# Kernel tuning notes

Hardware: AMD Instinct MI355X
Metric: run time of the kernel (lower is better)

The kernel has to match this reference:

```python
import jax, jax.numpy as jnp
import numpy as np

CHANNEL_N = 16
RESET_PROB = 0.5
ALIVE_THRESH = 0.1


def _perceive_kernel(c):
    # Faithful reproduction of the TF kernel construction:
    # stack([sobel_x, sobel_y, identity], axis=0) -> (3,3,3); expand_dims(-2);
    # repeat over channels -> (3,3,C,3). Depthwise conv treats axis0 as filter
    # height and the last axis as the channel multiplier (same as tf code).
    sx = jnp.array([[-1.0, 0.0, 1.0], [-2.0, 0.0, 2.0], [-1.0, 0.0, 1.0]], jnp.float32) / 8.0
    sy = sx.T
    ident = jnp.zeros((3, 3), jnp.float32).at[1, 1].set(1.0)
    k = jnp.stack([sx, sy, ident], axis=0)          # (3,3,3)
    k = jnp.repeat(k[:, :, None, :], c, axis=2)     # (3,3,C,3)
    # TF depthwise output ordering: out_ch = c*multiplier + m -> flatten (C,3)
    return k.reshape(3, 3, 1, c * 3)                # HWIO for grouped conv


def _alive_mask(x):
    # 3x3 max-pool (stride 1, SAME) on alpha channel, thresholded.
    alpha = x[..., 3:4]
    pooled = jax.lax.reduce_window(alpha, -jnp.inf, jax.lax.max,
                                   (1, 3, 3, 1), (1, 1, 1, 1), 'SAME')
    return pooled > ALIVE_THRESH


def setup_inputs() -> dict:
    key = jax.random.key(0)
    k1, k2, k3, k4, k5, k6 = jax.random.split(key, 6)
    B, H, W, C = 32, 256, 256, CHANNEL_N
    x = jax.random.uniform(k1, (B, H, W, C), dtype=jnp.float32)
    rand_mask = jax.random.uniform(k2, (B, H, W, 1), dtype=jnp.float32)
    W1 = jax.random.normal(k3, (3 * C, 128), dtype=jnp.float32) * 0.1
    b1 = jax.random.normal(k4, (128,), dtype=jnp.float32) * 0.1
    W2 = jax.random.normal(k5, (128, C), dtype=jnp.float32) * 0.1
    b2 = jax.random.normal(k6, (C,), dtype=jnp.float32) * 0.1
    return {"x": x, "rand_mask": rand_mask, "W1": W1, "b1": b1, "W2": W2, "b2": b2}


def reference(x, rand_mask, W1, b1, W2, b2):
    C = x.shape[-1]
    pre_update_mask = _alive_mask(x)
    # perceive: depthwise stencil conv, multiplier 3 -> (N,H,W,3C)
    kern = _perceive_kernel(C)
    y = jax.lax.conv_general_dilated(
        x, kern, window_strides=(1, 1), padding='SAME',
        dimension_numbers=('NHWC', 'HWIO', 'NHWC'), feature_group_count=C)
    # rule model: per-cell 1x1 MLP
    h = jax.nn.relu(jnp.einsum('nhwk,kd->nhwd', y, W1) + b1)
    dx = jnp.einsum('nhwd,dc->nhwc', h, W2) + b2
    # stochastic update mask
    upd = (rand_mask < RESET_PROB).astype(x.dtype)
    x = x + dx * upd
    post_update_mask = _alive_mask(x)
    life_mask = jnp.logical_and(pre_update_mask, post_update_mask).astype(x.dtype)
    return x * life_mask
```

## Files before the change

kernel.cpp:

```cpp
#include <hip/hip_runtime.h>

typedef __bf16 bf16x8 __attribute__((ext_vector_type(8)));
typedef float f32x4 __attribute__((ext_vector_type(4)));

#define XS_COLS 66
#define XS_CHP_B 32
#define XS_SLOT_B (XS_COLS * XS_CHP_B)
#define H_BYTES 16384
#define OFF_XS H_BYTES
#define SMEM_BYTES (H_BYTES + 4 * XS_SLOT_B)

__device__ __forceinline__ unsigned short bfbits(float f) {
    __bf16 b = (__bf16)f;
    return __builtin_bit_cast(unsigned short, b);
}

__global__ __launch_bounds__(256, 4) void nca_main(
    const float* __restrict__ x, const float* __restrict__ rm,
    const float* __restrict__ W1, const float* __restrict__ b1,
    const float* __restrict__ W2, const float* __restrict__ b2,
    float* __restrict__ out, unsigned int* __restrict__ am)
{
    __shared__ __align__(16) char smem[SMEM_BYTES];
    char* Hb  = smem;
    char* XSb = smem + OFF_XS;

    const int tid  = threadIdx.x;
    const int lane = tid & 63;
    const int wid  = tid >> 6;
    const int lrow = lane & 15;
    const int kg   = lane >> 4;
    const int kgh  = kg >> 1;
    const int kgl  = kg & 1;

    int raw = blockIdx.x;
    int wg  = (raw & 7) * 512 + (raw >> 3);
    int img = wg >> 7;
    int rem = wg & 127;
    int h0  = (rem >> 2) * 8;
    int w0  = (rem & 3) << 6;

    const size_t imgbase = (size_t)img * 65536;
    const int r = wid;

    bf16x8 wt[2][3];
    #pragma unroll
    for (int m = 0; m < 2; ++m) {
        int n = (r * 2 + m) * 16 + lrow;
        #pragma unroll
        for (int kk = 0; kk < 3; ++kk) {
            float c0, c1, c2;
            if (kk == 0) {
                c0 = kgh ? -0.25f : -0.125f; c1 = 0.f; c2 = kgh ? 0.25f : 0.125f;
            } else if (kk == 1) {
                c0 = -0.125f;
                c1 = kgh ? -0.25f  : 0.f;
                c2 = kgh ? -0.125f : 0.125f;
            } else {
                c0 = kgh ? 0.f : 0.125f; c1 = kgh ? 1.f : 0.25f; c2 = kgh ? 0.f : 0.125f;
            }
            bf16x8 v;
            #pragma unroll
            for (int j = 0; j < 8; ++j) {
                int ch = kgl * 8 + j;
                float wv = c0 * W1[(3 * ch + 0) * 128 + n]
                         + c1 * W1[(3 * ch + 1) * 128 + n]
                         + c2 * W1[(3 * ch + 2) * 128 + n];
                v[j] = (__bf16)wv;
            }
            wt[m][kk] = v;
        }
    }

    bf16x8 w2f[4];
    #pragma unroll
    for (int kk = 0; kk < 4; ++kk) {
        bf16x8 v;
        #pragma unroll
        for (int j = 0; j < 8; ++j)
            v[j] = (__bf16)W2[(kk * 32 + kg * 8 + j) * 16 + lrow];
        w2f[kk] = v;
    }

    f32x4 b1q[2];
    #pragma unroll
    for (int m = 0; m < 2; ++m)
        b1q[m] = *reinterpret_cast<const f32x4*>(b1 + (r * 2 + m) * 16 + kg * 4);
    const f32x4 b2q = *reinterpret_cast<const f32x4*>(b2 + kg * 4);

    for (int idx = tid; idx < 3 * 264; idx += 256) {
        int rr  = idx / 264;
        int q   = idx - rr * 264;
        int col = q >> 2, chq = q & 3;
        int gh = h0 - 1 + rr, gw = w0 + col - 1;
        int slot = (gh + 4) & 3;
        float4 v = make_float4(0.f, 0.f, 0.f, 0.f);
        if (gh >= 0 && gh < 256 && gw >= 0 && gw < 256)
            v = *reinterpret_cast<const float4*>(x + (imgbase + (size_t)gh * 256 + gw) * 16 + chq * 4);
        ushort4 qq = { bfbits(v.x), bfbits(v.y), bfbits(v.z), bfbits(v.w) };
        *reinterpret_cast<ushort4*>(XSb + slot * XS_SLOT_B + col * XS_CHP_B + chq * 8) = qq;
    }
    __syncthreads();

    for (int i = 0; i < 8; ++i) {
        int h = h0 + i;
        int sbm = ((h + 3) & 3) * XS_SLOT_B;
        int sb0 = ((h + 4) & 3) * XS_SLOT_B;
        int sbp = ((h + 5) & 3) * XS_SLOT_B;

        #pragma unroll
        for (int t = 0; t < 4; ++t) {
            int pxl = t * 16 + lrow;
            int colbase = (pxl + 1) * XS_CHP_B + kgl * 16;
            const char* a0p = XSb + sbm + colbase + (kgh ? 0 : -XS_CHP_B);
            const char* a1p = kgh ? (XSb + sb0 + colbase - XS_CHP_B) : (XSb + sbm + colbase + XS_CHP_B);
            const char* a2p = kgh ? (XSb + sbp + colbase)            : (XSb + sb0 + colbase + XS_CHP_B);
            bf16x8 bf0 = *reinterpret_cast<const bf16x8*>(a0p);
            bf16x8 bf1 = *reinterpret_cast<const bf16x8*>(a1p);
            bf16x8 bf2 = *reinterpret_cast<const bf16x8*>(a2p);
            f32x4 a0 = {0.f, 0.f, 0.f, 0.f}, a1 = {0.f, 0.f, 0.f, 0.f};
            a0 = __builtin_amdgcn_mfma_f32_16x16x32_bf16(wt[0][0], bf0, a0, 0, 0, 0);
            a1 = __builtin_amdgcn_mfma_f32_16x16x32_bf16(wt[1][0], bf0, a1, 0, 0, 0);
            a0 = __builtin_amdgcn_mfma_f32_16x16x32_bf16(wt[0][1], bf1, a0, 0, 0, 0);
            a1 = __builtin_amdgcn_mfma_f32_16x16x32_bf16(wt[1][1], bf1, a1, 0, 0, 0);
            a0 = __builtin_amdgcn_mfma_f32_16x16x32_bf16(wt[0][2], bf2, a0, 0, 0, 0);
            a1 = __builtin_amdgcn_mfma_f32_16x16x32_bf16(wt[1][2], bf2, a1, 0, 0, 0);
            #pragma unroll
            for (int m = 0; m < 2; ++m) {
                f32x4 hv = m ? a1 : a0;
                f32x4 bq = b1q[m];
                ushort4 q;
                q.x = bfbits(fmaxf(hv[0] + bq[0], 0.f));
                q.y = bfbits(fmaxf(hv[1] + bq[1], 0.f));
                q.z = bfbits(fmaxf(hv[2] + bq[2], 0.f));
                q.w = bfbits(fmaxf(hv[3] + bq[3], 0.f));
                int n0 = (r * 2 + m) * 16 + kg * 4;
                int chunk = (n0 >> 3) ^ (pxl & 7);
                *reinterpret_cast<ushort4*>(Hb + pxl * 256 + chunk * 16 + ((n0 >> 2) & 1) * 8) = q;
            }
        }
        __syncthreads();

        float4 sv0 = make_float4(0.f, 0.f, 0.f, 0.f), sv1 = make_float4(0.f, 0.f, 0.f, 0.f);
        const bool do_stage = (i < 7);
        const int gh2 = h + 2;
        if (do_stage) {
            int col0 = tid >> 2, chq0 = tid & 3;
            int gw = w0 + col0 - 1;
            if (gh2 < 256 && gw >= 0 && gw < 256)
                sv0 = *reinterpret_cast<const float4*>(x + (imgbase + (size_t)gh2 * 256 + gw) * 16 + chq0 * 4);
            if (tid < 8) {
                int col1 = 64 + (tid >> 2), gw1 = w0 + col1 - 1;
                if (gh2 < 256 && gw1 >= 0 && gw1 < 256)
                    sv1 = *reinterpret_cast<const float4*>(x + (imgbase + (size_t)gh2 * 256 + gw1) * 16 + (tid & 3) * 4);
            }
        }

        const int pxl2 = wid * 16 + lrow;
        f32x4 acc2 = {0.f, 0.f, 0.f, 0.f};
        #pragma unroll
        for (int kk = 0; kk < 4; ++kk) {
            int chunk = (4 * kk + kg) ^ (pxl2 & 7);
            bf16x8 hb = *reinterpret_cast<const bf16x8*>(Hb + pxl2 * 256 + chunk * 16);
            acc2 = __builtin_amdgcn_mfma_f32_16x16x32_bf16(w2f[kk], hb, acc2, 0, 0, 0);
        }

        size_t pix = imgbase + (size_t)h * 256 + w0 + pxl2;
        float upd = (rm[pix] < 0.5f) ? 1.f : 0.f;
        float4 xv = *reinterpret_cast<const float4*>(x + pix * 16 + kg * 4);
        float4 xn;
        xn.x = xv.x + (acc2[0] + b2q[0]) * upd;
        xn.y = xv.y + (acc2[1] + b2q[1]) * upd;
        xn.z = xv.z + (acc2[2] + b2q[2]) * upd;
        xn.w = xv.w + (acc2[3] + b2q[3]) * upd;
        *reinterpret_cast<float4*>(out + pix * 16 + kg * 4) = xn;
        if (kg == 0) {
            unsigned int av = ((unsigned int)bfbits(xv.w) << 16) | (unsigned int)bfbits(xn.w);
            am[pix] = av;
        }

        if (do_stage) {
            int slot = (gh2 + 4) & 3;
            {
                int col0 = tid >> 2, chq0 = tid & 3;
                ushort4 q = { bfbits(sv0.x), bfbits(sv0.y), bfbits(sv0.z), bfbits(sv0.w) };
                *reinterpret_cast<ushort4*>(XSb + slot * XS_SLOT_B + col0 * XS_CHP_B + chq0 * 8) = q;
            }
            if (tid < 8) {
                int col1 = 64 + (tid >> 2);
                ushort4 q = { bfbits(sv1.x), bfbits(sv1.y), bfbits(sv1.z), bfbits(sv1.w) };
                *reinterpret_cast<ushort4*>(XSb + slot * XS_SLOT_B + col1 * XS_CHP_B + (tid & 3) * 8) = q;
            }
        }
        __syncthreads();
    }
}

__global__ __launch_bounds__(256) void nca_life(
    const unsigned int* __restrict__ am, float* __restrict__ out)
{
    int q = blockIdx.x * 256 + threadIdx.x;
    int w = q & 255, hh = (q >> 8) & 255;
    float mn = -1e30f, mo = -1e30f;
    #pragma unroll
    for (int dh = -1; dh <= 1; ++dh) {
        int h2 = hh + dh;
        if (h2 < 0 || h2 > 255) continue;
        #pragma unroll
        for (int dw = -1; dw <= 1; ++dw) {
            int w2 = w + dw;
            if (w2 < 0 || w2 > 255) continue;
            unsigned int v = am[q + dh * 256 + dw];
            mn = fmaxf(mn, __uint_as_float(v << 16));
            mo = fmaxf(mo, __uint_as_float(v & 0xffff0000u));
        }
    }
    if (!(mo > 0.1f && mn > 0.1f)) {
        float4 z = make_float4(0.f, 0.f, 0.f, 0.f);
        float4* o = (float4*)(out + (size_t)q * 16);
        o[0] = z; o[1] = z; o[2] = z; o[3] = z;
    }
}

extern "C" void kernel_launch(void* const* d_in, const int* in_sizes, int n_in,
                              void* d_out, int out_size, void* d_ws, size_t ws_size,
                              hipStream_t stream) {
    (void)in_sizes; (void)n_in; (void)out_size; (void)ws_size;
    const float* x  = (const float*)d_in[0];
    const float* rm = (const float*)d_in[1];
    const float* W1 = (const float*)d_in[2];
    const float* b1 = (const float*)d_in[3];
    const float* W2 = (const float*)d_in[4];
    const float* b2 = (const float*)d_in[5];
    float* out = (float*)d_out;
    unsigned int* am = (unsigned int*)d_ws;

    nca_main<<<dim3(4096), dim3(256), 0, stream>>>(x, rm, W1, b1, W2, b2, out, am);
    nca_life<<<dim3(8192), dim3(256), 0, stream>>>(am, out);
}
```

Baseline: 127.4 us.

## Software-pipeline MLP layers with double-buffered hidden tile to halve barriers

Restructures the per-row loop so that layer 2 for row i-1 and layer 1 for row i run in the same iteration. The hidden-activation buffer is double-buffered and the x row ring grows from 4 to 8 slots, so each iteration needs one barrier instead of two. A final epilogue handles the last row. This roughly doubles the shared memory footprint to about 49KB per block, which may cut occupancy below the four blocks the launch bounds target.

Result: slower. 140.7 us (+10.5%).

```diff
diff --git a/kernel.cpp b/kernel.cpp
--- a/kernel.cpp
+++ b/kernel.cpp
@@ -6,9 +6,9 @@
 #define XS_COLS 66
 #define XS_CHP_B 32
 #define XS_SLOT_B (XS_COLS * XS_CHP_B)
-#define H_BYTES 16384
-#define OFF_XS H_BYTES
-#define SMEM_BYTES (H_BYTES + 4 * XS_SLOT_B)
+#define H_BUF_B 16384
+#define OFF_XS (2 * H_BUF_B)
+#define SMEM_BYTES (2 * H_BUF_B + 8 * XS_SLOT_B)
 
 __device__ __forceinline__ unsigned short bfbits(float f) {
     __bf16 b = (__bf16)f;
@@ -93,7 +93,7 @@
         int q   = idx - rr * 264;
         int col = q >> 2, chq = q & 3;
         int gh = h0 - 1 + rr, gw = w0 + col - 1;
-        int slot = (gh + 4) & 3;
+        int slot = (gh + 8) & 7;
         float4 v = make_float4(0.f, 0.f, 0.f, 0.f);
         if (gh >= 0 && gh < 256 && gw >= 0 && gw < 256)
             v = *reinterpret_cast<const float4*>(x + (imgbase + (size_t)gh * 256 + gw) * 16 + chq * 4);
@@ -104,46 +104,13 @@
 
     for (int i = 0; i < 8; ++i) {
         int h = h0 + i;
-        int sbm = ((h + 3) & 3) * XS_SLOT_B;
-        int sb0 = ((h + 4) & 3) * XS_SLOT_B;
-        int sbp = ((h + 5) & 3) * XS_SLOT_B;
-
-        #pragma unroll
-        for (int t = 0; t < 4; ++t) {
-            int pxl = t * 16 + lrow;
-            int colbase = (pxl + 1) * XS_CHP_B + kgl * 16;
-            const char* a0p = XSb + sbm + colbase + (kgh ? 0 : -XS_CHP_B);
-            const char* a1p = kgh ? (XSb + sb0 + colbase - XS_CHP_B) : (XSb + sbm + colbase + XS_CHP_B);
-            const char* a2p = kgh ? (XSb + sbp + colbase)            : (XSb + sb0 + colbase + XS_CHP_B);
-            bf16x8 bf0 = *reinterpret_cast<const bf16x8*>(a0p);
-            bf16x8 bf1 = *reinterpret_cast<const bf16x8*>(a1p);
-            bf16x8 bf2 = *reinterpret_cast<const bf16x8*>(a2p);
-            f32x4 a0 = {0.f, 0.f, 0.f, 0.f}, a1 = {0.f, 0.f, 0.f, 0.f};
-            a0 = __builtin_amdgcn_mfma_f32_16x16x32_bf16(wt[0][0], bf0, a0, 0, 0, 0);
-            a1 = __builtin_amdgcn_mfma_f32_16x16x32_bf16(wt[1][0], bf0, a1, 0, 0, 0);
-            a0 = __builtin_amdgcn_mfma_f32_16x16x32_bf16(wt[0][1], bf1, a0, 0, 0, 0);
-            a1 = __builtin_amdgcn_mfma_f32_16x16x32_bf16(wt[1][1], bf1, a1, 0, 0, 0);
-            a0 = __builtin_amdgcn_mfma_f32_16x16x32_bf16(wt[0][2], bf2, a0, 0, 0, 0);
-            a1 = __builtin_amdgcn_mfma_f32_16x16x32_bf16(wt[1][2], bf2, a1, 0, 0, 0);
-            #pragma unroll
-            for (int m = 0; m < 2; ++m) {
-                f32x4 hv = m ? a1 : a0;
-                f32x4 bq = b1q[m];
-                ushort4 q;
-                q.x = bfbits(fmaxf(hv[0] + bq[0], 0.f));
-                q.y = bfbits(fmaxf(hv[1] + bq[1], 0.f));
-                q.z = bfbits(fmaxf(hv[2] + bq[2], 0.f));
-                q.w = bfbits(fmaxf(hv[3] + bq[3], 0.f));
-                int n0 = (r * 2 + m) * 16 + kg * 4;
-                int chunk = (n0 >> 3) ^ (pxl & 7);
-                *reinterpret_cast<ushort4*>(Hb + pxl * 256 + chunk * 16 + ((n0 >> 2) & 1) * 8) = q;
-            }
-        }
-        __syncthreads();
-
-        float4 sv0 = make_float4(0.f, 0.f, 0.f, 0.f), sv1 = make_float4(0.f, 0.f, 0.f, 0.f);
+        int sbm = ((h + 7) & 7) * XS_SLOT_B;
+        int sb0 = (h & 7) * XS_SLOT_B;
+        int sbp = ((h + 1) & 7) * XS_SLOT_B;
+
         const bool do_stage = (i < 7);
         const int gh2 = h + 2;
+        float4 sv0 = make_float4(0.f, 0.f, 0.f, 0.f), sv1 = make_float4(0.f, 0.f, 0.f, 0.f);
         if (do_stage) {
             int col0 = tid >> 2, chq0 = tid & 3;
             int gw = w0 + col0 - 1;
@@ -156,18 +123,97 @@
             }
         }
 
+        if (i > 0) {
+            const char* Hr = Hb + ((i - 1) & 1) * H_BUF_B;
+            const int pxl2 = wid * 16 + lrow;
+            size_t pix = imgbase + (size_t)(h - 1) * 256 + w0 + pxl2;
+            float rmv = rm[pix];
+            float4 xv = *reinterpret_cast<const float4*>(x + pix * 16 + kg * 4);
+            f32x4 acc2 = {0.f, 0.f, 0.f, 0.f};
+            #pragma unroll
+            for (int kk = 0; kk < 4; ++kk) {
+                int chunk = (4 * kk + kg) ^ (pxl2 & 7);
+                bf16x8 hb = *reinterpret_cast<const bf16x8*>(Hr + pxl2 * 256 + chunk * 16);
+                acc2 = __builtin_amdgcn_mfma_f32_16x16x32_bf16(w2f[kk], hb, acc2, 0, 0, 0);
+            }
+            float upd = (rmv < 0.5f) ? 1.f : 0.f;
+            float4 xn;
+            xn.x = xv.x + (acc2[0] + b2q[0]) * upd;
+            xn.y = xv.y + (acc2[1] + b2q[1]) * upd;
+            xn.z = xv.z + (acc2[2] + b2q[2]) * upd;
+            xn.w = xv.w + (acc2[3] + b2q[3]) * upd;
+            *reinterpret_cast<float4*>(out + pix * 16 + kg * 4) = xn;
+            if (kg == 0) {
+                unsigned int av = ((unsigned int)bfbits(xv.w) << 16) | (unsigned int)bfbits(xn.w);
+                am[pix] = av;
+            }
+        }
+
+        if (do_stage) {
+            int slot = ((gh2) & 7);
+            {
+                int col0 = tid >> 2, chq0 = tid & 3;
+                ushort4 q = { bfbits(sv0.x), bfbits(sv0.y), bfbits(sv0.z), bfbits(sv0.w) };
+                *reinterpret_cast<ushort4*>(XSb + slot * XS_SLOT_B + col0 * XS_CHP_B + chq0 * 8) = q;
+            }
+            if (tid < 8) {
+                int col1 = 64 + (tid >> 2);
+                ushort4 q = { bfbits(sv1.x), bfbits(sv1.y), bfbits(sv1.z), bfbits(sv1.w) };
+                *reinterpret_cast<ushort4*>(XSb + slot * XS_SLOT_B + col1 * XS_CHP_B + (tid & 3) * 8) = q;
+            }
+        }
+
+        {
+            char* Hw = Hb + (i & 1) * H_BUF_B;
+            #pragma unroll
+            for (int t = 0; t < 4; ++t) {
+                int pxl = t * 16 + lrow;
+                int colbase = (pxl + 1) * XS_CHP_B + kgl * 16;
+                const char* a0p = XSb + sbm + colbase + (kgh ? 0 : -XS_CHP_B);
+                const char* a1p = kgh ? (XSb + sb0 + colbase - XS_CHP_B) : (XSb + sbm + colbase + XS_CHP_B);
+                const char* a2p = kgh ? (XSb + sbp + colbase)            : (XSb + sb0 + colbase + XS_CHP_B);
+                bf16x8 bf0 = *reinterpret_cast<const bf16x8*>(a0p);
+                bf16x8 bf1 = *reinterpret_cast<const bf16x8*>(a1p);
+                bf16x8 bf2 = *reinterpret_cast<const bf16x8*>(a2p);
+                f32x4 a0 = {0.f, 0.f, 0.f, 0.f}, a1 = {0.f, 0.f, 0.f, 0.f};
+                a0 = __builtin_amdgcn_mfma_f32_16x16x32_bf16(wt[0][0], bf0, a0, 0, 0, 0);
+                a1 = __builtin_amdgcn_mfma_f32_16x16x32_bf16(wt[1][0], bf0, a1, 0, 0, 0);
+                a0 = __builtin_amdgcn_mfma_f32_16x16x32_bf16(wt[0][1], bf1, a0, 0, 0, 0);
+                a1 = __builtin_amdgcn_mfma_f32_16x16x32_bf16(wt[1][1], bf1, a1, 0, 0, 0);
+                a0 = __builtin_amdgcn_mfma_f32_16x16x32_bf16(wt[0][2], bf2, a0, 0, 0, 0);
+                a1 = __builtin_amdgcn_mfma_f32_16x16x32_bf16(wt[1][2], bf2, a1, 0, 0, 0);
+                #pragma unroll
+                for (int m = 0; m < 2; ++m) {
+                    f32x4 hv = m ? a1 : a0;
+                    f32x4 bq = b1q[m];
+                    ushort4 q;
+                    q.x = bfbits(fmaxf(hv[0] + bq[0], 0.f));
+                    q.y = bfbits(fmaxf(hv[1] + bq[1], 0.f));
+                    q.z = bfbits(fmaxf(hv[2] + bq[2], 0.f));
+                    q.w = bfbits(fmaxf(hv[3] + bq[3], 0.f));
+                    int n0 = (r * 2 + m) * 16 + kg * 4;
+                    int chunk = (n0 >> 3) ^ (pxl & 7);
+                    *reinterpret_cast<ushort4*>(Hw + pxl * 256 + chunk * 16 + ((n0 >> 2) & 1) * 8) = q;
+                }
+            }
+        }
+        __syncthreads();
+    }
+
+    {
+        const char* Hr = Hb + H_BUF_B;
         const int pxl2 = wid * 16 + lrow;
+        size_t pix = imgbase + (size_t)(h0 + 7) * 256 + w0 + pxl2;
+        float rmv = rm[pix];
+        float4 xv = *reinterpret_cast<const float4*>(x + pix * 16 + kg * 4);
         f32x4 acc2 = {0.f, 0.f, 0.f, 0.f};
         #pragma unroll
         for (int kk = 0; kk < 4; ++kk) {
             int chunk = (4 * kk + kg) ^ (pxl2 & 7);
-            bf16x8 hb = *reinterpret_cast<const bf16x8*>(Hb + pxl2 * 256 + chunk * 16);
+            bf16x8 hb = *reinterpret_cast<const bf16x8*>(Hr + pxl2 * 256 + chunk * 16);
             acc2 = __builtin_amdgcn_mfma_f32_16x16x32_bf16(w2f[kk], hb, acc2, 0, 0, 0);
         }
-
-        size_t pix = imgbase + (size_t)h * 256 + w0 + pxl2;
-        float upd = (rm[pix] < 0.5f) ? 1.f : 0.f;
-        float4 xv = *reinterpret_cast<const float4*>(x + pix * 16 + kg * 4);
+        float upd = (rmv < 0.5f) ? 1.f : 0.f;
         float4 xn;
         xn.x = xv.x + (acc2[0] + b2q[0]) * upd;
         xn.y = xv.y + (acc2[1] + b2q[1]) * upd;
@@ -178,21 +224,6 @@
             unsigned int av = ((unsigned int)bfbits(xv.w) << 16) | (unsigned int)bfbits(xn.w);
             am[pix] = av;
         }
-
-        if (do_stage) {
-            int slot = (gh2 + 4) & 3;
-            {
-                int col0 = tid >> 2, chq0 = tid & 3;
-                ushort4 q = { bfbits(sv0.x), bfbits(sv0.y), bfbits(sv0.z), bfbits(sv0.w) };
-                *reinterpret_cast<ushort4*>(XSb + slot * XS_SLOT_B + col0 * XS_CHP_B + chq0 * 8) = q;
-            }
-            if (tid < 8) {
-                int col1 = 64 + (tid >> 2);
-                ushort4 q = { bfbits(sv1.x), bfbits(sv1.y), bfbits(sv1.z), bfbits(sv1.w) };
-                *reinterpret_cast<ushort4*>(XSb + slot * XS_SLOT_B + col1 * XS_CHP_B + (tid & 3) * 8) = q;
-            }
-        }
-        __syncthreads();
     }
 }
 
```
